# Optimization experiments

Measured on AMD Instinct MI355X. Metric: run time of the kernel, lower is better.

The kernel has to match this reference:

```python
import jax, jax.numpy as jnp
import numpy as np

N = 40000      # nodes
E = 640000     # edges (avg degree 16)
F = 128        # num_features
D = 128        # embedding_size
G = 128        # graphs in batch


def _glorot(key, shape):
    fan_in = shape[-1]
    return jax.random.normal(key, shape, jnp.float32) / np.float32(np.sqrt(fan_in))


def setup_inputs() -> dict:
    key = jax.random.key(0)
    ks = jax.random.split(key, 20)
    inp = {
        "x": jax.random.normal(ks[0], (N, F), jnp.float32),
        "edge_index": jax.random.randint(ks[1], (2, E), 0, N, dtype=jnp.int32),
        "batch_index": jnp.sort(jax.random.randint(ks[2], (N,), 0, G, dtype=jnp.int32)),
    }
    dims = [(D, F), (D, D), (D, D), (D, D)]
    for i, (dout, din) in enumerate(dims):
        inp[f"Wroot{i}"] = _glorot(ks[3 + 3 * i], (dout, din))
        inp[f"Wrel{i}"] = _glorot(ks[4 + 3 * i], (dout, din))
        inp[f"b{i}"] = jnp.zeros((dout,), jnp.float32)
    inp["Wout"] = _glorot(ks[18], (1, D))
    inp["bout"] = jnp.zeros((1,), jnp.float32)
    return inp


def _graph_conv(h, src, dst, Wroot, Wrel, b, num_nodes):
    # PyG GraphConv (aggr='add'): out_i = W_root x_i + W_rel * sum_{j->i} x_j + b
    # Linear commutes with the sum, so aggregate first then one dense GEMM.
    agg = jax.ops.segment_sum(h[src], dst, num_segments=num_nodes)  # [N, din]
    return h @ Wroot.T + agg @ Wrel.T + b


def reference(x, edge_index, batch_index,
              Wroot0, Wrel0, b0, Wroot1, Wrel1, b1,
              Wroot2, Wrel2, b2, Wroot3, Wrel3, b3,
              Wout, bout):
    src, dst = edge_index[0], edge_index[1]
    n = x.shape[0]
    h = x.astype(jnp.float32)
    layers = [(Wroot0, Wrel0, b0), (Wroot1, Wrel1, b1),
              (Wroot2, Wrel2, b2), (Wroot3, Wrel3, b3)]
    for Wr, Wn, b in layers:
        h = jax.nn.gelu(_graph_conv(h, src, dst, Wr, Wn, b, n), approximate=False)
        # dropout p=0.5 -> identity at eval time
    # global mean pool over graphs (gap)
    sums = jax.ops.segment_sum(h, batch_index, num_segments=G)        # [G, D]
    counts = jax.ops.segment_sum(jnp.ones((n,), jnp.float32), batch_index, num_segments=G)
    pooled = sums / jnp.maximum(counts, 1.0)[:, None]
    return pooled @ Wout.T + bout  # [G, 1]
```

## Files before the change

kernel.cpp:

```cpp
#include <hip/hip_runtime.h>
#include <hip/hip_bf16.h>

typedef __bf16 bf16x8 __attribute__((ext_vector_type(8)));
typedef float  f32x4  __attribute__((ext_vector_type(4)));

__device__ __forceinline__ float bf16lo(unsigned v) { return __uint_as_float(v << 16); }
__device__ __forceinline__ float bf16hi(unsigned v) { return __uint_as_float(v & 0xffff0000u); }


__global__ void degree_kernel(const int* __restrict__ dst, int* __restrict__ deg, int E) {
    int e = blockIdx.x * blockDim.x + threadIdx.x;
    if (e < E) atomicAdd(&deg[dst[e]], 1);
}

__global__ void scan_kernel(const int* __restrict__ deg, int* __restrict__ offsets,
                            int* __restrict__ cursor, int n) {
    __shared__ int wsum[16];
    __shared__ int carry_s;
    if (threadIdx.x == 0) carry_s = 0;
    __syncthreads();
    int lane = threadIdx.x & 63;
    int wave = threadIdx.x >> 6;
    for (int base = 0; base < n; base += 1024) {
        int i = base + threadIdx.x;
        int v = (i < n) ? deg[i] : 0;
        int s = v;
#pragma unroll
        for (int off = 1; off < 64; off <<= 1) {
            int t = __shfl_up(s, off, 64);
            if (lane >= off) s += t;
        }
        if (lane == 63) wsum[wave] = s;
        __syncthreads();
        if (wave == 0 && lane < 16) {
            int ws = wsum[lane];
            int ss = ws;
#pragma unroll
            for (int off = 1; off < 16; off <<= 1) {
                int t = __shfl_up(ss, off, 64);
                if (lane >= off) ss += t;
            }
            wsum[lane] = ss - ws;
        }
        __syncthreads();
        int excl = (s - v) + wsum[wave];
        int carry = carry_s;
        if (i < n) { offsets[i] = carry + excl; cursor[i] = carry + excl; }
        __syncthreads();
        if (threadIdx.x == 1023) carry_s = carry + excl + v;
        __syncthreads();
    }
    if (threadIdx.x == 0) offsets[n] = carry_s;
}

__global__ void scatter_kernel(const int* __restrict__ src, const int* __restrict__ dst,
                               int* __restrict__ cursor, int* __restrict__ sorted_src, int E) {
    int e = blockIdx.x * blockDim.x + threadIdx.x;
    if (e < E) {
        int d = dst[e];
        int pos = atomicAdd(&cursor[d], 1);
        sorted_src[pos] = src[e];
    }
}

__global__ void bounds_kernel(const int* __restrict__ batch, int* __restrict__ gstart,
                              int N, int G) {
    int g = blockIdx.x * blockDim.x + threadIdx.x;
    if (g <= G) {
        int lo = 0, hi = N;
        while (lo < hi) {
            int mid = (lo + hi) >> 1;
            if (batch[mid] < g) lo = mid + 1; else hi = mid;
        }
        gstart[g] = lo;
    }
}

__global__ void cvt_f32_to_bf16(const float* __restrict__ in,
                                __hip_bfloat16* __restrict__ out, int n) {
    int i = blockIdx.x * blockDim.x + threadIdx.x;
    if (i < n) out[i] = __float2bfloat16(in[i]);
}

__global__ void build_wcat(const float* __restrict__ Wr, const float* __restrict__ Wn,
                           __hip_bfloat16* __restrict__ Wcat) {
    int idx = blockIdx.x * blockDim.x + threadIdx.x;
    if (idx < 128 * 256) {
        int j = idx >> 8, k = idx & 255;
        float v = (k < 128) ? Wr[j * 128 + k] : Wn[j * 128 + (k - 128)];
        Wcat[idx] = __float2bfloat16(v);
    }
}


__global__ void agg_kernel(const __hip_bfloat16* __restrict__ h,
                           const int* __restrict__ offsets,
                           const int* __restrict__ sorted_src,
                           __hip_bfloat16* __restrict__ agg, int N) {
    int node = blockIdx.x * (blockDim.x >> 6) + (threadIdx.x >> 6);
    int lane = threadIdx.x & 63;
    if (node >= N) return;
    int s = offsets[node], e = offsets[node + 1];
    const unsigned* hu = (const unsigned*)h;
    float a0x = 0.f, a0y = 0.f, a1x = 0.f, a1y = 0.f;
    float a2x = 0.f, a2y = 0.f, a3x = 0.f, a3y = 0.f;
    int t = s;
    for (; t + 4 <= e; t += 4) {
        int n0 = sorted_src[t];
        int n1 = sorted_src[t + 1];
        int n2 = sorted_src[t + 2];
        int n3 = sorted_src[t + 3];
        unsigned v0 = hu[(size_t)n0 * 64 + lane];
        unsigned v1 = hu[(size_t)n1 * 64 + lane];
        unsigned v2 = hu[(size_t)n2 * 64 + lane];
        unsigned v3 = hu[(size_t)n3 * 64 + lane];
        a0x += bf16lo(v0); a0y += bf16hi(v0);
        a1x += bf16lo(v1); a1y += bf16hi(v1);
        a2x += bf16lo(v2); a2y += bf16hi(v2);
        a3x += bf16lo(v3); a3y += bf16hi(v3);
    }
    for (; t < e; ++t) {
        int nb = sorted_src[t];
        unsigned v = hu[(size_t)nb * 64 + lane];
        a0x += bf16lo(v); a0y += bf16hi(v);
    }
    float sx = (a0x + a1x) + (a2x + a3x);
    float sy = (a0y + a1y) + (a2y + a3y);
    __hip_bfloat162 o;
    o.x = __float2bfloat16(sx);
    o.y = __float2bfloat16(sy);
    *reinterpret_cast<__hip_bfloat162*>(&agg[(size_t)node * 128 + lane * 2]) = o;
}

__global__ void gemm_layer_kernel(const __hip_bfloat16* __restrict__ h,
                                  const __hip_bfloat16* __restrict__ agg,
                                  const __hip_bfloat16* __restrict__ Wcat,
                                  const float* __restrict__ bias,
                                  __hip_bfloat16* __restrict__ out, int N) {
    int wave = threadIdx.x >> 6;
    int lane = threadIdx.x & 63;
    int row0 = blockIdx.x * 128 + wave * 32;
    if (row0 >= N) return;

    int la  = lane & 15;
    int ke0 = (lane >> 4) * 8;

    int rA0 = row0 + la;       if (rA0 >= N) rA0 = N - 1;
    int rA1 = row0 + 16 + la;  if (rA1 >= N) rA1 = N - 1;

    f32x4 acc0[8] = {};
    f32x4 acc1[8] = {};

#pragma unroll
    for (int ks = 0; ks < 8; ++ks) {
        int k = ks * 32 + ke0;
        const __hip_bfloat16* base = (k < 128) ? h : agg;
        int kk = (k < 128) ? k : (k - 128);
        bf16x8 a0 = *reinterpret_cast<const bf16x8*>(&base[(size_t)rA0 * 128 + kk]);
        bf16x8 a1 = *reinterpret_cast<const bf16x8*>(&base[(size_t)rA1 * 128 + kk]);
#pragma unroll
        for (int n = 0; n < 8; ++n) {
            bf16x8 b = *reinterpret_cast<const bf16x8*>(&Wcat[(n * 16 + la) * 256 + k]);
            acc0[n] = __builtin_amdgcn_mfma_f32_16x16x32_bf16(a0, b, acc0[n], 0, 0, 0);
            acc1[n] = __builtin_amdgcn_mfma_f32_16x16x32_bf16(a1, b, acc1[n], 0, 0, 0);
        }
    }

    int orow = row0 + (lane >> 4) * 4;
#pragma unroll
    for (int n = 0; n < 8; ++n) {
        int col = n * 16 + la;
        float bv = bias[col];
#pragma unroll
        for (int j = 0; j < 4; ++j) {
            int r0 = orow + j;
            if (r0 < N) {
                float xv = acc0[n][j] + bv;
                float g = 0.5f * xv * (1.0f + erff(xv * 0.70710678118654752f));
                out[(size_t)r0 * 128 + col] = __float2bfloat16(g);
            }
            int r1 = orow + 16 + j;
            if (r1 < N) {
                float xv = acc1[n][j] + bv;
                float g = 0.5f * xv * (1.0f + erff(xv * 0.70710678118654752f));
                out[(size_t)r1 * 128 + col] = __float2bfloat16(g);
            }
        }
    }
}

__global__ void pool_partial(const __hip_bfloat16* __restrict__ h,
                             const int* __restrict__ batch,
                             float* __restrict__ pooled, int N) {
    int i0 = blockIdx.x * 64;
    int i1 = min(i0 + 64, N);
    if (i0 >= N) return;
    int lane = threadIdx.x;
    const unsigned* hu = (const unsigned*)h;
    float ax = 0.f, ay = 0.f;
    int cur = batch[i0];
    for (int i = i0; i < i1; ++i) {
        int b = batch[i];
        if (b != cur) {
            atomicAdd(&pooled[cur * 128 + lane * 2], ax);
            atomicAdd(&pooled[cur * 128 + lane * 2 + 1], ay);
            ax = 0.f; ay = 0.f; cur = b;
        }
        unsigned v = hu[(size_t)i * 64 + lane];
        ax += bf16lo(v); ay += bf16hi(v);
    }
    atomicAdd(&pooled[cur * 128 + lane * 2], ax);
    atomicAdd(&pooled[cur * 128 + lane * 2 + 1], ay);
}

__global__ void pool_finish(const float* __restrict__ pooled,
                            const int* __restrict__ gstart,
                            const float* __restrict__ Wout,
                            const float* __restrict__ bout,
                            float* __restrict__ out) {
    int g = blockIdx.x;
    int f = threadIdx.x;
    float cnt = (float)(gstart[g + 1] - gstart[g]);
    float v = pooled[g * 128 + f] * Wout[f];
    __shared__ float red[128];
    red[f] = v;
    __syncthreads();
    for (int off = 64; off > 0; off >>= 1) {
        if (f < off) red[f] += red[f + off];
        __syncthreads();
    }
    if (f == 0) out[g] = red[0] / fmaxf(cnt, 1.0f) + bout[0];
}


extern "C" void kernel_launch(void* const* d_in, const int* in_sizes, int n_in,
                              void* d_out, int out_size, void* d_ws, size_t ws_size,
                              hipStream_t stream) {
    const float* x          = (const float*)d_in[0];
    const int*   edge_index = (const int*)d_in[1];
    const int*   batch      = (const int*)d_in[2];
    const float* Wroot[4] = {(const float*)d_in[3], (const float*)d_in[6],
                             (const float*)d_in[9], (const float*)d_in[12]};
    const float* Wrel[4]  = {(const float*)d_in[4], (const float*)d_in[7],
                             (const float*)d_in[10], (const float*)d_in[13]};
    const float* bias[4]  = {(const float*)d_in[5], (const float*)d_in[8],
                             (const float*)d_in[11], (const float*)d_in[14]};
    const float* Wout = (const float*)d_in[15];
    const float* bout = (const float*)d_in[16];
    float* out = (float*)d_out;

    const int N = in_sizes[2];
    const int E = in_sizes[1] / 2;
    const int G = 128;
    const int* src = edge_index;
    const int* dst = edge_index + E;

    char* ws = (char*)d_ws;
    size_t o = 0;
    auto alloc = [&](size_t bytes) { void* p = ws + o; o += (bytes + 255) & ~(size_t)255; return p; };

    __hip_bfloat16* hx   = (__hip_bfloat16*)alloc((size_t)N * 128 * 2);
    __hip_bfloat16* hb0  = (__hip_bfloat16*)alloc((size_t)N * 128 * 2);
    __hip_bfloat16* hb1  = (__hip_bfloat16*)alloc((size_t)N * 128 * 2);
    __hip_bfloat16* agg  = (__hip_bfloat16*)alloc((size_t)N * 128 * 2);
    __hip_bfloat16* wcat[4];
    for (int l = 0; l < 4; ++l) wcat[l] = (__hip_bfloat16*)alloc(128 * 256 * 2);
    int* deg     = (int*)alloc((size_t)N * 4);
    int* offsets = (int*)alloc((size_t)(N + 1) * 4);
    int* cursor  = (int*)alloc((size_t)N * 4);
    int* sorted  = (int*)alloc((size_t)E * 4);
    int* gstart  = (int*)alloc((size_t)(G + 1) * 4);
    float* pooled = (float*)alloc((size_t)G * 128 * 4);

    hipMemsetAsync(deg, 0, (size_t)N * 4, stream);
    degree_kernel<<<(E + 255) / 256, 256, 0, stream>>>(dst, deg, E);
    scan_kernel<<<1, 1024, 0, stream>>>(deg, offsets, cursor, N);
    scatter_kernel<<<(E + 255) / 256, 256, 0, stream>>>(src, dst, cursor, sorted, E);
    bounds_kernel<<<1, 256, 0, stream>>>(batch, gstart, N, G);

    cvt_f32_to_bf16<<<(N * 128 + 255) / 256, 256, 0, stream>>>(x, hx, N * 128);
    for (int l = 0; l < 4; ++l)
        build_wcat<<<(128 * 256 + 255) / 256, 256, 0, stream>>>(Wroot[l], Wrel[l], wcat[l]);

    __hip_bfloat16* hin = hx;
    __hip_bfloat16* houts[4] = {hb0, hb1, hb0, hb1};
    for (int l = 0; l < 4; ++l) {
        agg_kernel<<<(N + 3) / 4, 256, 0, stream>>>(hin, offsets, sorted, agg, N);
        gemm_layer_kernel<<<(N + 127) / 128, 256, 0, stream>>>(hin, agg, wcat[l], bias[l], houts[l], N);
        hin = houts[l];
    }

    hipMemsetAsync(pooled, 0, (size_t)G * 128 * 4, stream);
    pool_partial<<<(N + 63) / 64, 64, 0, stream>>>(hin, batch, pooled, N);
    pool_finish<<<G, 128, 0, stream>>>(pooled, gstart, Wout, bout, out);
}
```

Before: 493.1 us.

## Deepen agg unroll, restructure GEMM tiling, and use tanh GELU approximation

```diff
diff --git a/kernel.cpp b/kernel.cpp
--- a/kernel.cpp
+++ b/kernel.cpp
@@ -6,6 +6,13 @@
 
 __device__ __forceinline__ float bf16lo(unsigned v) { return __uint_as_float(v << 16); }
 __device__ __forceinline__ float bf16hi(unsigned v) { return __uint_as_float(v & 0xffff0000u); }
+
+__device__ __forceinline__ float gelu_f(float x) {
+    float t = 0.7978845608028654f * (x + 0.044715f * x * x * x);
+    float e = __expf(2.0f * t);
+    float th = 1.0f - 2.0f / (1.0f + e);
+    return 0.5f * x * (1.0f + th);
+}
 
 
 __global__ void degree_kernel(const int* __restrict__ dst, int* __restrict__ deg, int E) {
@@ -105,11 +112,31 @@
     float a0x = 0.f, a0y = 0.f, a1x = 0.f, a1y = 0.f;
     float a2x = 0.f, a2y = 0.f, a3x = 0.f, a3y = 0.f;
     int t = s;
-    for (; t + 4 <= e; t += 4) {
-        int n0 = sorted_src[t];
-        int n1 = sorted_src[t + 1];
-        int n2 = sorted_src[t + 2];
-        int n3 = sorted_src[t + 3];
+    for (; t + 8 <= e; t += 8) {
+        int n0 = sorted_src[t],     n1 = sorted_src[t + 1];
+        int n2 = sorted_src[t + 2], n3 = sorted_src[t + 3];
+        int n4 = sorted_src[t + 4], n5 = sorted_src[t + 5];
+        int n6 = sorted_src[t + 6], n7 = sorted_src[t + 7];
+        unsigned v0 = hu[(size_t)n0 * 64 + lane];
+        unsigned v1 = hu[(size_t)n1 * 64 + lane];
+        unsigned v2 = hu[(size_t)n2 * 64 + lane];
+        unsigned v3 = hu[(size_t)n3 * 64 + lane];
+        unsigned v4 = hu[(size_t)n4 * 64 + lane];
+        unsigned v5 = hu[(size_t)n5 * 64 + lane];
+        unsigned v6 = hu[(size_t)n6 * 64 + lane];
+        unsigned v7 = hu[(size_t)n7 * 64 + lane];
+        a0x += bf16lo(v0); a0y += bf16hi(v0);
+        a1x += bf16lo(v1); a1y += bf16hi(v1);
+        a2x += bf16lo(v2); a2y += bf16hi(v2);
+        a3x += bf16lo(v3); a3y += bf16hi(v3);
+        a0x += bf16lo(v4); a0y += bf16hi(v4);
+        a1x += bf16lo(v5); a1y += bf16hi(v5);
+        a2x += bf16lo(v6); a2y += bf16hi(v6);
+        a3x += bf16lo(v7); a3y += bf16hi(v7);
+    }
+    if (t + 4 <= e) {
+        int n0 = sorted_src[t],     n1 = sorted_src[t + 1];
+        int n2 = sorted_src[t + 2], n3 = sorted_src[t + 3];
         unsigned v0 = hu[(size_t)n0 * 64 + lane];
         unsigned v1 = hu[(size_t)n1 * 64 + lane];
         unsigned v2 = hu[(size_t)n2 * 64 + lane];
@@ -118,10 +145,18 @@
         a1x += bf16lo(v1); a1y += bf16hi(v1);
         a2x += bf16lo(v2); a2y += bf16hi(v2);
         a3x += bf16lo(v3); a3y += bf16hi(v3);
-    }
-    for (; t < e; ++t) {
-        int nb = sorted_src[t];
-        unsigned v = hu[(size_t)nb * 64 + lane];
+        t += 4;
+    }
+    if (t + 2 <= e) {
+        int n0 = sorted_src[t], n1 = sorted_src[t + 1];
+        unsigned v0 = hu[(size_t)n0 * 64 + lane];
+        unsigned v1 = hu[(size_t)n1 * 64 + lane];
+        a0x += bf16lo(v0); a0y += bf16hi(v0);
+        a1x += bf16lo(v1); a1y += bf16hi(v1);
+        t += 2;
+    }
+    if (t < e) {
+        unsigned v = hu[(size_t)sorted_src[t] * 64 + lane];
         a0x += bf16lo(v); a0y += bf16hi(v);
     }
     float sx = (a0x + a1x) + (a2x + a3x);
@@ -139,51 +174,50 @@
                                   __hip_bfloat16* __restrict__ out, int N) {
     int wave = threadIdx.x >> 6;
     int lane = threadIdx.x & 63;
-    int row0 = blockIdx.x * 128 + wave * 32;
+    int row0 = (blockIdx.x >> 1) * 128;
+    int cg   = ((blockIdx.x & 1) << 2) | wave;
     if (row0 >= N) return;
 
     int la  = lane & 15;
     int ke0 = (lane >> 4) * 8;
-
-    int rA0 = row0 + la;       if (rA0 >= N) rA0 = N - 1;
-    int rA1 = row0 + 16 + la;  if (rA1 >= N) rA1 = N - 1;
-
-    f32x4 acc0[8] = {};
-    f32x4 acc1[8] = {};
-
-#pragma unroll
-    for (int ks = 0; ks < 8; ++ks) {
-        int k = ks * 32 + ke0;
-        const __hip_bfloat16* base = (k < 128) ? h : agg;
-        int kk = (k < 128) ? k : (k - 128);
-        bf16x8 a0 = *reinterpret_cast<const bf16x8*>(&base[(size_t)rA0 * 128 + kk]);
-        bf16x8 a1 = *reinterpret_cast<const bf16x8*>(&base[(size_t)rA1 * 128 + kk]);
-#pragma unroll
-        for (int n = 0; n < 8; ++n) {
-            bf16x8 b = *reinterpret_cast<const bf16x8*>(&Wcat[(n * 16 + la) * 256 + k]);
-            acc0[n] = __builtin_amdgcn_mfma_f32_16x16x32_bf16(a0, b, acc0[n], 0, 0, 0);
-            acc1[n] = __builtin_amdgcn_mfma_f32_16x16x32_bf16(a1, b, acc1[n], 0, 0, 0);
-        }
-    }
-
-    int orow = row0 + (lane >> 4) * 4;
-#pragma unroll
-    for (int n = 0; n < 8; ++n) {
-        int col = n * 16 + la;
-        float bv = bias[col];
+    int col = cg * 16 + la;
+
+    bf16x8 b[8];
+#pragma unroll
+    for (int ks = 0; ks < 8; ++ks)
+        b[ks] = *reinterpret_cast<const bf16x8*>(&Wcat[(size_t)col * 256 + ks * 32 + ke0]);
+
+    float bv = bias[col];
+
+    f32x4 acc[8];
+#pragma unroll
+    for (int m = 0; m < 8; ++m) {
+        int r = row0 + m * 16 + la;
+        if (r >= N) r = N - 1;
+        const __hip_bfloat16* hr = &h[(size_t)r * 128];
+        const __hip_bfloat16* ar = &agg[(size_t)r * 128];
+        bf16x8 a[8];
+#pragma unroll
+        for (int ks = 0; ks < 4; ++ks) {
+            a[ks]     = *reinterpret_cast<const bf16x8*>(&hr[ks * 32 + ke0]);
+            a[ks + 4] = *reinterpret_cast<const bf16x8*>(&ar[ks * 32 + ke0]);
+        }
+        f32x4 c = {};
+#pragma unroll
+        for (int ks = 0; ks < 8; ++ks)
+            c = __builtin_amdgcn_mfma_f32_16x16x32_bf16(a[ks], b[ks], c, 0, 0, 0);
+        acc[m] = c;
+    }
+
+    int r0 = row0 + (lane >> 4) * 4;
+#pragma unroll
+    for (int m = 0; m < 8; ++m) {
 #pragma unroll
         for (int j = 0; j < 4; ++j) {
-            int r0 = orow + j;
-            if (r0 < N) {
-                float xv = acc0[n][j] + bv;
-                float g = 0.5f * xv * (1.0f + erff(xv * 0.70710678118654752f));
-                out[(size_t)r0 * 128 + col] = __float2bfloat16(g);
-            }
-            int r1 = orow + 16 + j;
-            if (r1 < N) {
-                float xv = acc1[n][j] + bv;
-                float g = 0.5f * xv * (1.0f + erff(xv * 0.70710678118654752f));
-                out[(size_t)r1 * 128 + col] = __float2bfloat16(g);
+            int r = r0 + m * 16 + j;
+            if (r < N) {
+                float xv = acc[m][j] + bv;
+                out[(size_t)r * 128 + col] = __float2bfloat16(gelu_f(xv));
             }
         }
     }
@@ -286,7 +320,7 @@
     __hip_bfloat16* houts[4] = {hb0, hb1, hb0, hb1};
     for (int l = 0; l < 4; ++l) {
         agg_kernel<<<(N + 3) / 4, 256, 0, stream>>>(hin, offsets, sorted, agg, N);
-        gemm_layer_kernel<<<(N + 127) / 128, 256, 0, stream>>>(hin, agg, wcat[l], bias[l], houts[l], N);
+        gemm_layer_kernel<<<((N + 127) / 128) * 2, 256, 0, stream>>>(hin, agg, wcat[l], bias[l], houts[l], N);
         hin = houts[l];
     }
 
```

After: 458.2 us. 7.1% less time.
